# Kernel tuning notes

Measured on AMD Instinct MI355X. Metric: run time of the kernel, lower is better.

The kernel has to match this reference:

```python
import jax, jax.numpy as jnp
import numpy as np

N = 4096
IN_F = 256
H = 4
D = 64
WIN = 128
HALF = WIN // 2
TAU = 0.5
TOP_K = 32


def setup_inputs() -> dict:
    key = jax.random.key(0)
    ks = jax.random.split(key, 5)
    node_features = jax.random.normal(ks[0], (N, IN_F), dtype=jnp.float32)
    s = 1.0 / np.sqrt(IN_F)
    Wq = jax.random.normal(ks[1], (IN_F, H * D), dtype=jnp.float32) * s
    bq = jax.random.normal(ks[2], (H * D,), dtype=jnp.float32) * 0.01
    Wk = jax.random.normal(ks[3], (IN_F, H * D), dtype=jnp.float32) * s
    bk = jax.random.normal(ks[4], (H * D,), dtype=jnp.float32) * 0.01
    num_nodes_per_graph = jnp.full((8,), 512, dtype=jnp.int32)  # 8 graphs x 512 = N
    return {"node_features": node_features, "Wq": Wq, "bq": bq, "Wk": Wk,
            "bk": bk, "num_nodes_per_graph": num_nodes_per_graph, "num_relation": 1}


def reference(node_features, Wq, bq, Wk, bk, num_nodes_per_graph, num_relation):
    n = node_features.shape[0]
    scale = jnp.sqrt(jnp.asarray(D, node_features.dtype))

    Q = (node_features @ Wq + bq).reshape(n, H, D)
    K = (node_features @ Wk + bk).reshape(n, H, D)

    # segment boundaries (graph.num_nodes.repeat(num_relation) -> cumsum -> searchsorted)
    segment = jnp.tile(num_nodes_per_graph, num_relation)
    cum = jnp.cumsum(segment)
    i = jnp.arange(n)
    pos = jnp.searchsorted(cum, i, side='right')
    seg_start = jnp.where(pos == 0, 0, cum[jnp.maximum(pos - 1, 0)])
    seg_end = cum[jnp.minimum(pos, cum.shape[0] - 1)]

    start = jnp.maximum(seg_start, i - HALF)  # [N]
    end = jnp.minimum(seg_end, i + HALF)      # [N]

    gather_idx = start[:, None] + jnp.arange(WIN)[None, :]
    valid = gather_idx < end[:, None]
    gi = jnp.clip(gather_idx, 0, n - 1)
    Kw = jnp.where(valid[:, :, None, None], K[gi], 0.0)

    # scores over full window incl. zero padding (faithful: original does not mask softmax)
    scores = jnp.einsum('nhd,nmhd->nhm', Q, Kw) / scale / TAU
    attn = jax.nn.softmax(scores, axis=-1).mean(axis=1)

    # scatter attention rows into dense N x N (padded slots add 0)
    output = jnp.zeros((n, n), node_features.dtype).at[i[:, None], gi].add(
        jnp.where(valid, attn, 0.0))

    # gumbel_softmax_top_k(output, tau, hard=self.k) -> hard=True (k truthy)
    g = jax.random.gumbel(jax.random.key(42), output.shape, output.dtype)
    y_soft = jax.nn.softmax((output + g) / TAU, axis=-1)
    topk_idx = jax.lax.top_k(output, TOP_K)[1]                  # [N, TOP_K]
    y_hard = jnp.zeros_like(output).at[i[:, None], topk_idx].set(1.0)
    y = jax.lax.stop_gradient(y_hard - y_soft) + y_soft
    return y
```

## Files before the change

### kernel.cpp

```cpp
#include <hip/hip_runtime.h>

#define NF   256
#define HD   256
#define NH   4
#define DH   64
#define WINS 128
#define HALFW 64
#define TOPK 32
#define GR   8

__global__ __launch_bounds__(512) void qk_gemm_kernel(
    const float* __restrict__ X,
    const float* __restrict__ Wq, const float* __restrict__ bq,
    const float* __restrict__ Wk, const float* __restrict__ bk,
    float* __restrict__ Qb, float* __restrict__ Kb, int n)
{
    const int t   = threadIdx.x;
    const int col = t & 255;
    const bool isK = (t >= 256);
    const float* W   = isK ? Wk : Wq;
    const float* bia = isK ? bk : bq;
    float*       Out = isK ? Kb : Qb;

    const int rowBase = blockIdx.x * GR;
    const float* Xb = X + (size_t)rowBase * NF;

    float acc[GR];
#pragma unroll
    for (int r = 0; r < GR; ++r) acc[r] = 0.f;

    for (int k = 0; k < NF; k += 4) {
        float w0 = W[(size_t)(k + 0) * HD + col];
        float w1 = W[(size_t)(k + 1) * HD + col];
        float w2 = W[(size_t)(k + 2) * HD + col];
        float w3 = W[(size_t)(k + 3) * HD + col];
#pragma unroll
        for (int r = 0; r < GR; ++r) {
            float4 f = *(const float4*)(Xb + r * NF + k);
            acc[r] += f.x * w0 + f.y * w1 + f.z * w2 + f.w * w3;
        }
    }
    float bias = bia[col];
#pragma unroll
    for (int r = 0; r < GR; ++r)
        Out[(size_t)(rowBase + r) * HD + col] = acc[r] + bias;
}

__global__ __launch_bounds__(256) void attn_topk_kernel(
    const float* __restrict__ Q,
    const float* __restrict__ K,
    const int* __restrict__ nnpg, int n_graphs,
    const int* __restrict__ nrel,
    float* __restrict__ out, int n)
{
    const int i    = blockIdx.x;
    const int t    = threadIdx.x;
    const int wave = t >> 6;
    const int lane = t & 63;

    __shared__ float sc[NH][WINS];
    __shared__ float pr[NH][WINS];
    __shared__ float attnv[WINS];
    __shared__ float slotval[WINS];

    int R = nrel[0];
    int total = n_graphs * R;
    int seg_start = 0, seg_end = n;
    int cum = 0;
    for (int e = 0; e < total; ++e) {
        int sz = nnpg[e % n_graphs];
        int nc = cum + sz;
        if (i < nc) { seg_start = cum; seg_end = nc; break; }
        cum = nc;
    }
    const int start = max(seg_start, i - HALFW);
    const int end   = min(seg_end,   i + HALFW);
    const int win   = end - start;

    const float4 q4 = *(const float4*)(Q + (size_t)i * HD + lane * 4);

#pragma unroll 4
    for (int j = 0; j < 32; ++j) {
        int row = wave + 4 * j;
        float v = 0.f;
        if (row < win) {
            float4 k4 = *(const float4*)(K + (size_t)(start + row) * HD + lane * 4);
            v = q4.x * k4.x + q4.y * k4.y + q4.z * k4.z + q4.w * k4.w;
        }
        v += __shfl_xor(v, 1);
        v += __shfl_xor(v, 2);
        v += __shfl_xor(v, 4);
        v += __shfl_xor(v, 8);
        if ((lane & 15) == 0)
            sc[lane >> 4][row] = v * 0.25f;
    }
    __syncthreads();

    {
        float v0 = sc[wave][lane], v1 = sc[wave][lane + 64];
        float mx = fmaxf(v0, v1);
#pragma unroll
        for (int off = 32; off > 0; off >>= 1) mx = fmaxf(mx, __shfl_xor(mx, off));
        float e0 = expf(v0 - mx), e1 = expf(v1 - mx);
        float sm = e0 + e1;
#pragma unroll
        for (int off = 32; off > 0; off >>= 1) sm += __shfl_xor(sm, off);
        pr[wave][lane]      = e0 / sm;
        pr[wave][lane + 64] = e1 / sm;
    }
    __syncthreads();

    if (t < WINS) {
        float a = 0.25f * (pr[0][t] + pr[1][t] + pr[2][t] + pr[3][t]);
        attnv[t] = (t < win) ? a : -1.0f;
    }
    __syncthreads();

    if (t < WINS) {
        float v = attnv[t];
        int cnt = 0;
#pragma unroll
        for (int j4 = 0; j4 < WINS / 4; ++j4) {
            float4 a4 = *(const float4*)&attnv[j4 * 4];
            int jb = j4 * 4;
            cnt += (a4.x > v) || (a4.x == v && (jb + 0) < t);
            cnt += (a4.y > v) || (a4.y == v && (jb + 1) < t);
            cnt += (a4.z > v) || (a4.z == v && (jb + 2) < t);
            cnt += (a4.w > v) || (a4.w == v && (jb + 3) < t);
        }
        slotval[t] = (t < win && cnt < TOPK) ? 1.0f : 0.0f;
    }
    __syncthreads();

    float4* orow = (float4*)(out + (size_t)i * n);
    const int n4 = n >> 2;
    for (int c4 = t; c4 < n4; c4 += 256) {
        int c = c4 << 2;
        float4 v4 = make_float4(0.f, 0.f, 0.f, 0.f);
        if (c + 3 >= start && c < end) {
            int o = c - start;
            if (o     >= 0 && o     < WINS) v4.x = slotval[o];
            if (o + 1 >= 0 && o + 1 < WINS) v4.y = slotval[o + 1];
            if (o + 2 >= 0 && o + 2 < WINS) v4.z = slotval[o + 2];
            if (o + 3 >= 0 && o + 3 < WINS) v4.w = slotval[o + 3];
        }
        orow[c4] = v4;
    }
}

extern "C" void kernel_launch(void* const* d_in, const int* in_sizes, int n_in,
                              void* d_out, int out_size, void* d_ws, size_t ws_size,
                              hipStream_t stream)
{
    const float* X  = (const float*)d_in[0];
    const float* Wq = (const float*)d_in[1];
    const float* bq = (const float*)d_in[2];
    const float* Wk = (const float*)d_in[3];
    const float* bk = (const float*)d_in[4];
    const int* nnpg = (const int*)d_in[5];
    const int* nrel = (const int*)d_in[6];

    const int n = in_sizes[0] / NF;
    const int n_graphs = in_sizes[5];

    float* Qb = (float*)d_ws;
    float* Kb = Qb + (size_t)n * HD;
    float* out = (float*)d_out;

    qk_gemm_kernel<<<n / GR, 512, 0, stream>>>(X, Wq, bq, Wk, bk, Qb, Kb, n);
    attn_topk_kernel<<<n, 256, 0, stream>>>(Qb, Kb, nnpg, n_graphs, nrel, out, n);
}
```

Baseline: 157.1 us.

## Store K transposed and compute window scores per lane without shuffles

The QK projection now writes K in transposed layout (feature-major) and splits Q and K into separate grid rows, staging the X tile in shared memory. The attention kernel loads Q into shared memory and each lane computes full dot products for two window positions by walking K's transposed columns, which are coalesced across lanes. This removes the shuffle-reduction loop and the score staging buffer. In exchange each lane issues serial dependent loads per head dimension, and the transposed writes in the GEMM are strided.

```diff
diff --git a/kernel.cpp b/kernel.cpp
--- a/kernel.cpp
+++ b/kernel.cpp
@@ -9,46 +9,60 @@
 #define TOPK 32
 #define GR   8
 
-__global__ __launch_bounds__(512) void qk_gemm_kernel(
+__global__ __launch_bounds__(256) void qk_gemm_kernel(
     const float* __restrict__ X,
     const float* __restrict__ Wq, const float* __restrict__ bq,
     const float* __restrict__ Wk, const float* __restrict__ bk,
-    float* __restrict__ Qb, float* __restrict__ Kb, int n)
+    float* __restrict__ Qb, float* __restrict__ Kt, int n)
 {
-    const int t   = threadIdx.x;
-    const int col = t & 255;
-    const bool isK = (t >= 256);
+    const bool isK = (blockIdx.y != 0);
     const float* W   = isK ? Wk : Wq;
     const float* bia = isK ? bk : bq;
-    float*       Out = isK ? Kb : Qb;
 
+    __shared__ float feat[GR][NF];
     const int rowBase = blockIdx.x * GR;
-    const float* Xb = X + (size_t)rowBase * NF;
+    const int t = threadIdx.x;
+
+    {
+        const float4* src = (const float4*)(X + (size_t)rowBase * NF);
+        float4* dst = (float4*)&feat[0][0];
+        dst[t]       = src[t];
+        dst[t + 256] = src[t + 256];
+    }
+    __syncthreads();
 
     float acc[GR];
 #pragma unroll
     for (int r = 0; r < GR; ++r) acc[r] = 0.f;
 
+#pragma unroll 4
     for (int k = 0; k < NF; k += 4) {
-        float w0 = W[(size_t)(k + 0) * HD + col];
-        float w1 = W[(size_t)(k + 1) * HD + col];
-        float w2 = W[(size_t)(k + 2) * HD + col];
-        float w3 = W[(size_t)(k + 3) * HD + col];
+        float w0 = W[(size_t)(k + 0) * HD + t];
+        float w1 = W[(size_t)(k + 1) * HD + t];
+        float w2 = W[(size_t)(k + 2) * HD + t];
+        float w3 = W[(size_t)(k + 3) * HD + t];
 #pragma unroll
         for (int r = 0; r < GR; ++r) {
-            float4 f = *(const float4*)(Xb + r * NF + k);
+            float4 f = *(const float4*)&feat[r][k];
             acc[r] += f.x * w0 + f.y * w1 + f.z * w2 + f.w * w3;
         }
     }
-    float bias = bia[col];
+    float bias = bia[t];
+
+    if (!isK) {
 #pragma unroll
-    for (int r = 0; r < GR; ++r)
-        Out[(size_t)(rowBase + r) * HD + col] = acc[r] + bias;
+        for (int r = 0; r < GR; ++r)
+            Qb[(size_t)(rowBase + r) * HD + t] = acc[r] + bias;
+    } else {
+        float4* o = (float4*)(Kt + (size_t)t * n + rowBase);
+        o[0] = make_float4(acc[0] + bias, acc[1] + bias, acc[2] + bias, acc[3] + bias);
+        o[1] = make_float4(acc[4] + bias, acc[5] + bias, acc[6] + bias, acc[7] + bias);
+    }
 }
 
 __global__ __launch_bounds__(256) void attn_topk_kernel(
     const float* __restrict__ Q,
-    const float* __restrict__ K,
+    const float* __restrict__ KT,
     const int* __restrict__ nnpg, int n_graphs,
     const int* __restrict__ nrel,
     float* __restrict__ out, int n)
@@ -58,7 +72,7 @@
     const int wave = t >> 6;
     const int lane = t & 63;
 
-    __shared__ float sc[NH][WINS];
+    __shared__ float qs[HD];
     __shared__ float pr[NH][WINS];
     __shared__ float attnv[WINS];
     __shared__ float slotval[WINS];
@@ -77,37 +91,37 @@
     const int end   = min(seg_end,   i + HALFW);
     const int win   = end - start;
 
-    const float4 q4 = *(const float4*)(Q + (size_t)i * HD + lane * 4);
-
-#pragma unroll 4
-    for (int j = 0; j < 32; ++j) {
-        int row = wave + 4 * j;
-        float v = 0.f;
-        if (row < win) {
-            float4 k4 = *(const float4*)(K + (size_t)(start + row) * HD + lane * 4);
-            v = q4.x * k4.x + q4.y * k4.y + q4.z * k4.z + q4.w * k4.w;
-        }
-        v += __shfl_xor(v, 1);
-        v += __shfl_xor(v, 2);
-        v += __shfl_xor(v, 4);
-        v += __shfl_xor(v, 8);
-        if ((lane & 15) == 0)
-            sc[lane >> 4][row] = v * 0.25f;
-    }
+    qs[t] = Q[(size_t)i * HD + t];
     __syncthreads();
 
-    {
-        float v0 = sc[wave][lane], v1 = sc[wave][lane + 64];
-        float mx = fmaxf(v0, v1);
+    const bool v0 = (lane      < win);
+    const bool v1 = (lane + 64 < win);
+    const int  j0 = v0 ? (start + lane)      : start;
+    const int  j1 = v1 ? (start + lane + 64) : start;
+
+    const float* kcol = KT + (size_t)(wave * DH) * n;
+    const float* qh   = qs + wave * DH;
+
+    float a0 = 0.f, a1 = 0.f;
+#pragma unroll 8
+    for (int d = 0; d < DH; ++d) {
+        float qd = qh[d];
+        const float* col = kcol + (size_t)d * n;
+        a0 += qd * col[j0];
+        a1 += qd * col[j1];
+    }
+    a0 = v0 ? a0 * 0.25f : 0.f;
+    a1 = v1 ? a1 * 0.25f : 0.f;
+
+    float mx = fmaxf(a0, a1);
 #pragma unroll
-        for (int off = 32; off > 0; off >>= 1) mx = fmaxf(mx, __shfl_xor(mx, off));
-        float e0 = expf(v0 - mx), e1 = expf(v1 - mx);
-        float sm = e0 + e1;
+    for (int off = 32; off > 0; off >>= 1) mx = fmaxf(mx, __shfl_xor(mx, off));
+    float e0 = expf(a0 - mx), e1 = expf(a1 - mx);
+    float sm = e0 + e1;
 #pragma unroll
-        for (int off = 32; off > 0; off >>= 1) sm += __shfl_xor(sm, off);
-        pr[wave][lane]      = e0 / sm;
-        pr[wave][lane + 64] = e1 / sm;
-    }
+    for (int off = 32; off > 0; off >>= 1) sm += __shfl_xor(sm, off);
+    pr[wave][lane]      = e0 / sm;
+    pr[wave][lane + 64] = e1 / sm;
     __syncthreads();
 
     if (t < WINS) {
@@ -164,9 +178,10 @@
     const int n_graphs = in_sizes[5];
 
     float* Qb = (float*)d_ws;
-    float* Kb = Qb + (size_t)n * HD;
+    float* Kt = Qb + (size_t)n * HD;
     float* out = (float*)d_out;
 
-    qk_gemm_kernel<<<n / GR, 512, 0, stream>>>(X, Wq, bq, Wk, bk, Qb, Kb, n);
-    attn_topk_kernel<<<n, 256, 0, stream>>>(Qb, Kb, nnpg, n_graphs, nrel, out, n);
+    dim3 gg(n / GR, 2);
+    qk_gemm_kernel<<<gg, 256, 0, stream>>>(X, Wq, bq, Wk, bk, Qb, Kt, n);
+    attn_topk_kernel<<<n, 256, 0, stream>>>(Qb, Kt, nnpg, n_graphs, nrel, out, n);
 }
```

Result: slower. 161.2 us (+2.6%).

## Fuse output zero-fill into QK GEMM and batch four rows per attention block

Applied to the files above, without the earlier changes.

Zeroing of the dense N x N output moves into the projection GEMM kernel, which also stages weight chunks in LDS and processes 16 rows per block. The attention kernel now handles four query rows per block, reusing each loaded K row across them, and handles padded window slots analytically in the softmax. It writes only the top-k ones instead of rewriting whole output rows. This removes the per-row full-width store loop and redundant K reads, but it relies on kernel ordering so the zero-fill completes before the scattered writes.

```diff
diff --git a/kernel.cpp b/kernel.cpp
--- a/kernel.cpp
+++ b/kernel.cpp
@@ -1,49 +1,74 @@
 #include <hip/hip_runtime.h>
 
-#define NF   256
-#define HD   256
-#define NH   4
-#define DH   64
-#define WINS 128
+#define NF    256
+#define HD    256
+#define NH    4
+#define DH    64
+#define WINS  128
 #define HALFW 64
-#define TOPK 32
-#define GR   8
-
-__global__ __launch_bounds__(512) void qk_gemm_kernel(
+#define TOPK  32
+#define GROWS 16
+#define KCH   64
+#define NB    4
+#define UMAX  132
+
+__global__ __launch_bounds__(256) void qk_gemm_fill_kernel(
     const float* __restrict__ X,
     const float* __restrict__ Wq, const float* __restrict__ bq,
     const float* __restrict__ Wk, const float* __restrict__ bk,
-    float* __restrict__ Qb, float* __restrict__ Kb, int n)
+    float* __restrict__ Qb, float* __restrict__ Kb,
+    float4* __restrict__ outz, int total4, int per_block, int n)
 {
-    const int t   = threadIdx.x;
-    const int col = t & 255;
-    const bool isK = (t >= 256);
+    __shared__ float lw[KCH * HD];
+    const int t = threadIdx.x;
+    const bool isK = (blockIdx.y != 0);
     const float* W   = isK ? Wk : Wq;
     const float* bia = isK ? bk : bq;
     float*       Out = isK ? Kb : Qb;
 
-    const int rowBase = blockIdx.x * GR;
-    const float* Xb = X + (size_t)rowBase * NF;
-
-    float acc[GR];
-#pragma unroll
-    for (int r = 0; r < GR; ++r) acc[r] = 0.f;
-
-    for (int k = 0; k < NF; k += 4) {
-        float w0 = W[(size_t)(k + 0) * HD + col];
-        float w1 = W[(size_t)(k + 1) * HD + col];
-        float w2 = W[(size_t)(k + 2) * HD + col];
-        float w3 = W[(size_t)(k + 3) * HD + col];
-#pragma unroll
-        for (int r = 0; r < GR; ++r) {
-            float4 f = *(const float4*)(Xb + r * NF + k);
-            acc[r] += f.x * w0 + f.y * w1 + f.z * w2 + f.w * w3;
-        }
-    }
-    float bias = bia[col];
-#pragma unroll
-    for (int r = 0; r < GR; ++r)
-        Out[(size_t)(rowBase + r) * HD + col] = acc[r] + bias;
+    const int rowBase = __builtin_amdgcn_readfirstlane(blockIdx.x * GROWS);
+    const float* Xs = X + (size_t)rowBase * NF;
+
+    float acc[GROWS];
+#pragma unroll
+    for (int r = 0; r < GROWS; ++r) acc[r] = 0.f;
+
+    for (int k0 = 0; k0 < NF; k0 += KCH) {
+        __syncthreads();
+        {
+            const float4* wsrc = (const float4*)(W + (size_t)k0 * HD);
+            float4* ldst = (float4*)lw;
+#pragma unroll
+            for (int j = 0; j < (KCH * HD / 4) / 256; ++j)
+                ldst[j * 256 + t] = wsrc[j * 256 + t];
+        }
+        __syncthreads();
+#pragma unroll 8
+        for (int kk = 0; kk < KCH; kk += 4) {
+            float w0 = lw[(kk + 0) * HD + t];
+            float w1 = lw[(kk + 1) * HD + t];
+            float w2 = lw[(kk + 2) * HD + t];
+            float w3 = lw[(kk + 3) * HD + t];
+#pragma unroll
+            for (int r = 0; r < GROWS; ++r) {
+                float4 xv = *(const float4*)(Xs + r * NF + k0 + kk);
+                acc[r] += xv.x * w0 + xv.y * w1 + xv.z * w2 + xv.w * w3;
+            }
+        }
+    }
+
+    const float bv = bia[t];
+#pragma unroll
+    for (int r = 0; r < GROWS; ++r)
+        Out[(size_t)(rowBase + r) * HD + t] = acc[r] + bv;
+
+    const int bflat = blockIdx.y * gridDim.x + blockIdx.x;
+    const size_t base = (size_t)bflat * per_block;
+    const float4 z = make_float4(0.f, 0.f, 0.f, 0.f);
+    for (int j = t; j < per_block; j += 256) {
+        size_t g = base + j;
+        if (g < (size_t)total4) outz[g] = z;
+    }
 }
 
 __global__ __launch_bounds__(256) void attn_topk_kernel(
@@ -53,99 +78,107 @@
     const int* __restrict__ nrel,
     float* __restrict__ out, int n)
 {
-    const int i    = blockIdx.x;
     const int t    = threadIdx.x;
     const int wave = t >> 6;
     const int lane = t & 63;
-
-    __shared__ float sc[NH][WINS];
-    __shared__ float pr[NH][WINS];
-    __shared__ float attnv[WINS];
-    __shared__ float slotval[WINS];
-
-    int R = nrel[0];
-    int total = n_graphs * R;
-    int seg_start = 0, seg_end = n;
-    int cum = 0;
-    for (int e = 0; e < total; ++e) {
-        int sz = nnpg[e % n_graphs];
-        int nc = cum + sz;
-        if (i < nc) { seg_start = cum; seg_end = nc; break; }
-        cum = nc;
-    }
-    const int start = max(seg_start, i - HALFW);
-    const int end   = min(seg_end,   i + HALFW);
-    const int win   = end - start;
-
-    const float4 q4 = *(const float4*)(Q + (size_t)i * HD + lane * 4);
-
-#pragma unroll 4
-    for (int j = 0; j < 32; ++j) {
-        int row = wave + 4 * j;
-        float v = 0.f;
-        if (row < win) {
-            float4 k4 = *(const float4*)(K + (size_t)(start + row) * HD + lane * 4);
-            v = q4.x * k4.x + q4.y * k4.y + q4.z * k4.z + q4.w * k4.w;
-        }
-        v += __shfl_xor(v, 1);
-        v += __shfl_xor(v, 2);
-        v += __shfl_xor(v, 4);
-        v += __shfl_xor(v, 8);
-        if ((lane & 15) == 0)
-            sc[lane >> 4][row] = v * 0.25f;
+    const int i0   = blockIdx.x * NB;
+
+    __shared__ float sc[NB][NH][UMAX];
+    __shared__ float attnv[NB][WINS];
+
+    int st[NB], en[NB];
+    {
+        int R = nrel[0];
+        int total = n_graphs * R;
+#pragma unroll
+        for (int nn = 0; nn < NB; ++nn) {
+            int i = i0 + nn, ss = 0, se = n, cum = 0;
+            for (int e = 0; e < total; ++e) {
+                int sz = nnpg[e % n_graphs];
+                int nc = cum + sz;
+                if (i >= cum && i < nc) { ss = cum; se = nc; }
+                cum = nc;
+            }
+            st[nn] = max(ss, i - HALFW);
+            en[nn] = min(se, i + HALFW);
+        }
+    }
+    const int u0 = st[0];
+    const int U  = en[NB - 1] - u0;
+
+    float4 q4[NB];
+#pragma unroll
+    for (int nn = 0; nn < NB; ++nn)
+        q4[nn] = *(const float4*)(Q + (size_t)(i0 + nn) * HD + 4 * lane);
+
+    const int h = lane >> 4;
+
+    for (int r = wave; r < U; r += 4) {
+        float4 k4 = *(const float4*)(K + (size_t)(u0 + r) * HD + 4 * lane);
+#pragma unroll
+        for (int nn = 0; nn < NB; ++nn) {
+            float d = q4[nn].x * k4.x + q4[nn].y * k4.y +
+                      q4[nn].z * k4.z + q4[nn].w * k4.w;
+            d += __shfl_xor(d, 1);
+            d += __shfl_xor(d, 2);
+            d += __shfl_xor(d, 4);
+            d += __shfl_xor(d, 8);
+            if ((lane & 15) == 0) sc[nn][h][r] = d * 0.25f;
+        }
     }
     __syncthreads();
 
-    {
-        float v0 = sc[wave][lane], v1 = sc[wave][lane + 64];
-        float mx = fmaxf(v0, v1);
-#pragma unroll
-        for (int off = 32; off > 0; off >>= 1) mx = fmaxf(mx, __shfl_xor(mx, off));
-        float e0 = expf(v0 - mx), e1 = expf(v1 - mx);
-        float sm = e0 + e1;
-#pragma unroll
-        for (int off = 32; off > 0; off >>= 1) sm += __shfl_xor(sm, off);
-        pr[wave][lane]      = e0 / sm;
-        pr[wave][lane + 64] = e1 / sm;
-    }
-    __syncthreads();
-
-    if (t < WINS) {
-        float a = 0.25f * (pr[0][t] + pr[1][t] + pr[2][t] + pr[3][t]);
-        attnv[t] = (t < win) ? a : -1.0f;
-    }
-    __syncthreads();
-
-    if (t < WINS) {
-        float v = attnv[t];
-        int cnt = 0;
-#pragma unroll
-        for (int j4 = 0; j4 < WINS / 4; ++j4) {
-            float4 a4 = *(const float4*)&attnv[j4 * 4];
-            int jb = j4 * 4;
-            cnt += (a4.x > v) || (a4.x == v && (jb + 0) < t);
-            cnt += (a4.y > v) || (a4.y == v && (jb + 1) < t);
-            cnt += (a4.z > v) || (a4.z == v && (jb + 2) < t);
-            cnt += (a4.w > v) || (a4.w == v && (jb + 3) < t);
-        }
-        slotval[t] = (t < win && cnt < TOPK) ? 1.0f : 0.0f;
-    }
-    __syncthreads();
-
-    float4* orow = (float4*)(out + (size_t)i * n);
-    const int n4 = n >> 2;
-    for (int c4 = t; c4 < n4; c4 += 256) {
-        int c = c4 << 2;
-        float4 v4 = make_float4(0.f, 0.f, 0.f, 0.f);
-        if (c + 3 >= start && c < end) {
-            int o = c - start;
-            if (o     >= 0 && o     < WINS) v4.x = slotval[o];
-            if (o + 1 >= 0 && o + 1 < WINS) v4.y = slotval[o + 1];
-            if (o + 2 >= 0 && o + 2 < WINS) v4.z = slotval[o + 2];
-            if (o + 3 >= 0 && o + 3 < WINS) v4.w = slotval[o + 3];
-        }
-        orow[c4] = v4;
-    }
+    const int nn = wave;
+    int stn = st[0], enn = en[0];
+    if (nn == 1) { stn = st[1]; enn = en[1]; }
+    if (nn == 2) { stn = st[2]; enn = en[2]; }
+    if (nn == 3) { stn = st[3]; enn = en[3]; }
+    const int off = stn - u0;
+    const int win = enn - stn;
+
+    float mean0 = 0.f, mean1 = 0.f;
+#pragma unroll
+    for (int hh = 0; hh < NH; ++hh) {
+        float s0 = (lane      < win) ? sc[nn][hh][off + lane]      : -1e30f;
+        float s1 = (lane + 64 < win) ? sc[nn][hh][off + lane + 64] : -1e30f;
+        float m = fmaxf(s0, s1);
+#pragma unroll
+        for (int o = 32; o > 0; o >>= 1) m = fmaxf(m, __shfl_xor(m, o));
+        if (win < WINS) m = fmaxf(m, 0.f);
+        float e0 = (lane      < win) ? expf(s0 - m) : 0.f;
+        float e1 = (lane + 64 < win) ? expf(s1 - m) : 0.f;
+        float ssum = e0 + e1;
+#pragma unroll
+        for (int o = 32; o > 0; o >>= 1) ssum += __shfl_xor(ssum, o);
+        ssum += (float)(WINS - win) * expf(-m);
+        float inv = 1.f / ssum;
+        mean0 += e0 * inv;
+        mean1 += e1 * inv;
+    }
+    const float w0v = (lane      < win) ? mean0 * 0.25f : -1.0f;
+    const float w1v = (lane + 64 < win) ? mean1 * 0.25f : -1.0f;
+    attnv[nn][lane]      = w0v;
+    attnv[nn][lane + 64] = w1v;
+
+    int cnt0 = 0, cnt1 = 0;
+    const int s0i = lane, s1i = lane + 64;
+#pragma unroll
+    for (int j4 = 0; j4 < WINS / 4; ++j4) {
+        float4 a4 = *(const float4*)&attnv[nn][j4 * 4];
+        int jb = j4 * 4;
+        cnt0 += (a4.x > w0v) || (a4.x == w0v && (jb + 0) < s0i);
+        cnt0 += (a4.y > w0v) || (a4.y == w0v && (jb + 1) < s0i);
+        cnt0 += (a4.z > w0v) || (a4.z == w0v && (jb + 2) < s0i);
+        cnt0 += (a4.w > w0v) || (a4.w == w0v && (jb + 3) < s0i);
+        cnt1 += (a4.x > w1v) || (a4.x == w1v && (jb + 0) < s1i);
+        cnt1 += (a4.y > w1v) || (a4.y == w1v && (jb + 1) < s1i);
+        cnt1 += (a4.z > w1v) || (a4.z == w1v && (jb + 2) < s1i);
+        cnt1 += (a4.w > w1v) || (a4.w == w1v && (jb + 3) < s1i);
+    }
+
+    float* orow = out + (size_t)(i0 + nn) * n;
+    if (s0i < win && cnt0 < TOPK) orow[stn + s0i] = 1.0f;
+    if (s1i < win && cnt1 < TOPK) orow[stn + s1i] = 1.0f;
 }
 
 extern "C" void kernel_launch(void* const* d_in, const int* in_sizes, int n_in,
@@ -167,6 +200,14 @@
     float* Kb = Qb + (size_t)n * HD;
     float* out = (float*)d_out;
 
-    qk_gemm_kernel<<<n / GR, 512, 0, stream>>>(X, Wq, bq, Wk, bk, Qb, Kb, n);
-    attn_topk_kernel<<<n, 256, 0, stream>>>(Qb, Kb, nnpg, n_graphs, nrel, out, n);
+    const int gx = n / GROWS;
+    const int nblocks = gx * 2;
+    const int total4 = out_size >> 2;
+    const int per_block = (total4 + nblocks - 1) / nblocks;
+
+    dim3 gg(gx, 2);
+    qk_gemm_fill_kernel<<<gg, 256, 0, stream>>>(X, Wq, bq, Wk, bk, Qb, Kb,
+                                                (float4*)out, total4, per_block, n);
+
+    attn_topk_kernel<<<n / NB, 256, 0, stream>>>(Qb, Kb, nnpg, n_graphs, nrel, out, n);
 }
```

Measured after the change: 309.4 us. 1.97x slower.

## Retile QK projection GEMM into 8x4 register tiles with scalar X loads

Applied to the files above, without the earlier changes.

The Q/K projection kernel now gives each thread an 8-row by 4-column register tile. X rows are read through a wave-uniform pointer, so they can become scalar loads, and W rows are read as float4. Q and K are split across a second grid dimension. The aim is more reuse of each W load across rows and fewer vector memory instructions. The attention kernel's score loop unroll also goes from 4 to 8. The cost is higher register pressure per thread.

```diff
diff --git a/kernel.cpp b/kernel.cpp
--- a/kernel.cpp
+++ b/kernel.cpp
@@ -1,49 +1,60 @@
 #include <hip/hip_runtime.h>
 
-#define NF   256
-#define HD   256
-#define NH   4
-#define DH   64
-#define WINS 128
+#define NF    256
+#define HD    256
+#define NH    4
+#define DH    64
+#define WINS  128
 #define HALFW 64
-#define TOPK 32
-#define GR   8
+#define TOPK  32
+#define GROWS 32
 
-__global__ __launch_bounds__(512) void qk_gemm_kernel(
+__global__ __launch_bounds__(256) void qk_gemm_kernel(
     const float* __restrict__ X,
     const float* __restrict__ Wq, const float* __restrict__ bq,
     const float* __restrict__ Wk, const float* __restrict__ bk,
     float* __restrict__ Qb, float* __restrict__ Kb, int n)
 {
-    const int t   = threadIdx.x;
-    const int col = t & 255;
-    const bool isK = (t >= 256);
+    const int t    = threadIdx.x;
+    const int wave = t >> 6;
+    const int lane = t & 63;
+    const bool isK = (blockIdx.y != 0);
     const float* W   = isK ? Wk : Wq;
     const float* bia = isK ? bk : bq;
     float*       Out = isK ? Kb : Qb;
 
-    const int rowBase = blockIdx.x * GR;
-    const float* Xb = X + (size_t)rowBase * NF;
+    const int r0  = blockIdx.x * GROWS + wave * 8;
+    const int r0s = __builtin_amdgcn_readfirstlane(r0);
+    const float* Xs = X + (size_t)r0s * NF;
 
-    float acc[GR];
+    float4 acc[8];
 #pragma unroll
-    for (int r = 0; r < GR; ++r) acc[r] = 0.f;
+    for (int r = 0; r < 8; ++r) acc[r] = make_float4(0.f, 0.f, 0.f, 0.f);
 
-    for (int k = 0; k < NF; k += 4) {
-        float w0 = W[(size_t)(k + 0) * HD + col];
-        float w1 = W[(size_t)(k + 1) * HD + col];
-        float w2 = W[(size_t)(k + 2) * HD + col];
-        float w3 = W[(size_t)(k + 3) * HD + col];
+    for (int k = 0; k < NF; k += 8) {
+        float4 wv[8];
 #pragma unroll
-        for (int r = 0; r < GR; ++r) {
-            float4 f = *(const float4*)(Xb + r * NF + k);
-            acc[r] += f.x * w0 + f.y * w1 + f.z * w2 + f.w * w3;
+        for (int u = 0; u < 8; ++u)
+            wv[u] = *(const float4*)(W + (size_t)(k + u) * HD + 4 * lane);
+#pragma unroll
+        for (int u = 0; u < 8; ++u) {
+#pragma unroll
+            for (int r = 0; r < 8; ++r) {
+                float xk = Xs[r * NF + k + u];
+                acc[r].x += xk * wv[u].x;
+                acc[r].y += xk * wv[u].y;
+                acc[r].z += xk * wv[u].z;
+                acc[r].w += xk * wv[u].w;
+            }
         }
     }
-    float bias = bia[col];
+
+    const float4 bv = *(const float4*)(bia + 4 * lane);
 #pragma unroll
-    for (int r = 0; r < GR; ++r)
-        Out[(size_t)(rowBase + r) * HD + col] = acc[r] + bias;
+    for (int r = 0; r < 8; ++r) {
+        acc[r].x += bv.x; acc[r].y += bv.y; acc[r].z += bv.z; acc[r].w += bv.w;
+        *(float4*)(Out + (size_t)(r0 + r) * HD + 4 * lane) = acc[r];
+    }
 }
 
 __global__ __launch_bounds__(256) void attn_topk_kernel(
@@ -79,7 +90,7 @@
 
     const float4 q4 = *(const float4*)(Q + (size_t)i * HD + lane * 4);
 
-#pragma unroll 4
+#pragma unroll 8
     for (int j = 0; j < 32; ++j) {
         int row = wave + 4 * j;
         float v = 0.f;
@@ -167,6 +178,8 @@
     float* Kb = Qb + (size_t)n * HD;
     float* out = (float*)d_out;
 
-    qk_gemm_kernel<<<n / GR, 512, 0, stream>>>(X, Wq, bq, Wk, bk, Qb, Kb, n);
+    dim3 gg(n / GROWS, 2);
+    qk_gemm_kernel<<<gg, 256, 0, stream>>>(X, Wq, bq, Wk, bk, Qb, Kb, n);
+
     attn_topk_kernel<<<n, 256, 0, stream>>>(Qb, Kb, nnpg, n_graphs, nrel, out, n);
 }
```

Measured after the change: 155.8 us. No clear change (-0.8%).
